# Kernel tuning notes

Hardware: AMD Instinct MI355X
Metric: run time of the kernel (lower is better)

## Reference

```python
import jax, jax.numpy as jnp
import numpy as np

N = 100000   # nodes
E = 800000   # edges
F = 64       # num_features == hidden_dim
D = 64       # hidden_dim
L = 3        # num_gc_layers
NG = 512     # num graphs in batch
BN_EPS = 1e-5


def setup_inputs() -> dict:
    key = jax.random.key(0)
    ks = jax.random.split(key, 16)
    s = 0.05
    return {
        "x": jax.random.normal(ks[0], (N, F), jnp.float32),
        "edge_index": jax.random.randint(ks[1], (2, E), 0, N),
        "batch": jnp.sort(jax.random.randint(ks[2], (N,), 0, NG)),
        "W1": jax.random.normal(ks[3], (L, F, D), jnp.float32) * s,
        "b1": jnp.zeros((L, D), jnp.float32),
        "W2": jax.random.normal(ks[4], (L, D, D), jnp.float32) * s,
        "b2": jnp.zeros((L, D), jnp.float32),
        "gin_eps": jnp.zeros((L,), jnp.float32),
        "gin_bias": jnp.zeros((L, D), jnp.float32),
        "bn_gamma": jnp.ones((L, D), jnp.float32),
        "bn_beta": jnp.zeros((L, D), jnp.float32),
        "Wp1": jax.random.normal(ks[5], (L * D, L * D), jnp.float32) * s,
        "bp1": jnp.zeros((L * D,), jnp.float32),
        "Wp2": jax.random.normal(ks[6], (L * D, L * D), jnp.float32) * s,
        "bp2": jnp.zeros((L * D,), jnp.float32),
    }


def reference(x, edge_index, batch, W1, b1, W2, b2, gin_eps, gin_bias,
              bn_gamma, bn_beta, Wp1, bp1, Wp2, bp2):
    row, col = edge_index[0], edge_index[1]
    h = x
    xs = []
    for i in range(L):
        # sparse adj @ h : sum over incoming edges (adj[row, col] = 1)
        agg = jax.ops.segment_sum(h[col], row, num_segments=N)
        z = (1.0 + gin_eps[i]) * h + agg
        # GIN internal MLP: Linear -> ReLU -> Linear -> ReLU
        z = jax.nn.relu(z @ W1[i] + b1[i])
        z = jax.nn.relu(z @ W2[i] + b2[i])
        # conv bias + relu (outer F.relu in Encoder is idempotent)
        z = jax.nn.relu(z + gin_bias[i])
        # BatchNorm1d, training mode: batch stats over nodes, biased variance
        mean = jnp.mean(z, axis=0)
        var = jnp.mean(jnp.square(z - mean), axis=0)
        h = (z - mean) * jax.lax.rsqrt(var + BN_EPS) * bn_gamma[i] + bn_beta[i]
        xs.append(h)
    # per-layer global add pool over graphs, then concat -> [NG, L*D]
    pooled = jnp.concatenate(
        [jax.ops.segment_sum(xi, batch, num_segments=NG) for xi in xs], axis=1)
    # projection head: Linear -> ReLU -> Linear
    y = jax.nn.relu(pooled @ Wp1 + bp1) @ Wp2 + bp2
    return y
```

## Files before the change

### kernel.cpp

```cpp
#include <hip/hip_runtime.h>

#define N_NODES 100000
#define N_EDGES 800000
#define DF 64
#define NGRAPH 512
#define LDIM 192
#define BN_EPS 1e-5
#define NTILES 6250
#define GIN_GRID 782
#define NWT (GIN_GRID * 8)
#define NPACKS 12500
#define COLS_CAP 2600000
#define NBUCK 782
#define BCAP 2048
#define NBLK 128
#define CHUNK 6250
#define REGION_CAP 6144
#define PROJ_ROWS 8

typedef __attribute__((ext_vector_type(8))) short bf16x8;
typedef __attribute__((ext_vector_type(4))) float f32x4;

__device__ inline short f2bf(float x) {
    union { float f; unsigned u; } v; v.f = x;
    unsigned r = v.u + 0x7fff + ((v.u >> 16) & 1);
    return (short)(r >> 16);
}
__device__ inline float bf2f(unsigned short u) {
    union { unsigned u; float f; } v; v.u = ((unsigned)u) << 16; return v.f;
}
__device__ inline float bflo(unsigned u) {
    union { unsigned x; float f; } v; v.x = u << 16; return v.f;
}
__device__ inline float bfhi(unsigned u) {
    union { unsigned x; float f; } v; v.x = u & 0xffff0000u; return v.f;
}

__global__ __launch_bounds__(256) void x2bf_kernel(
    const float* __restrict__ x, unsigned short* __restrict__ xb)
{
    int i = blockIdx.x * 256 + threadIdx.x;
    const int total = N_NODES * DF / 8;
    if (i >= total) return;
    const float4* src = (const float4*)(x + (size_t)i * 8);
    float4 a = src[0], b = src[1];
    unsigned short u0 = (unsigned short)f2bf(a.x), u1 = (unsigned short)f2bf(a.y);
    unsigned short u2 = (unsigned short)f2bf(a.z), u3 = (unsigned short)f2bf(a.w);
    unsigned short u4 = (unsigned short)f2bf(b.x), u5 = (unsigned short)f2bf(b.y);
    unsigned short u6 = (unsigned short)f2bf(b.z), u7 = (unsigned short)f2bf(b.w);
    uint4 o;
    o.x = (unsigned)u0 | ((unsigned)u1 << 16);
    o.y = (unsigned)u2 | ((unsigned)u3 << 16);
    o.z = (unsigned)u4 | ((unsigned)u5 << 16);
    o.w = (unsigned)u6 | ((unsigned)u7 << 16);
    ((uint4*)xb)[i] = o;
}

__global__ __launch_bounds__(256) void blk_hist_kernel(
    const int* __restrict__ ei, int* __restrict__ hist)
{
    __shared__ int hh[NBUCK];
    int blk = blockIdx.x, tid = threadIdx.x;
    for (int i = tid; i < NBUCK; i += 256) hh[i] = 0;
    __syncthreads();
    int start = blk * CHUNK, end = min(start + CHUNK, N_EDGES);
    for (int e = start + tid; e < end; e += 256)
        atomicAdd(&hh[ei[e] >> 7], 1);
    __syncthreads();
    for (int i = tid; i < NBUCK; i += 256) hist[blk * NBUCK + i] = hh[i];
}

__global__ __launch_bounds__(NBLK) void blk_scan_kernel(
    const int* __restrict__ hist, int* __restrict__ pos, int* __restrict__ cnt)
{
    __shared__ int buf[NBLK];
    int k = blockIdx.x, b = threadIdx.x;
    int v = hist[b * NBUCK + k];
    buf[b] = v;
    __syncthreads();
    for (int o = 1; o < NBLK; o <<= 1) {
        int t = (b >= o) ? buf[b - o] : 0;
        __syncthreads();
        buf[b] += t;
        __syncthreads();
    }
    pos[b * NBUCK + k] = buf[b] - v;
    if (b == NBLK - 1) cnt[k] = buf[b];
}

__global__ __launch_bounds__(256) void place_kernel(
    const int* __restrict__ ei, const int* __restrict__ pos,
    unsigned* __restrict__ bucketData)
{
    __shared__ int cursor[NBUCK];
    int blk = blockIdx.x, tid = threadIdx.x;
    for (int i = tid; i < NBUCK; i += 256) cursor[i] = pos[blk * NBUCK + i];
    __syncthreads();
    int start = blk * CHUNK, end = min(start + CHUNK, N_EDGES);
    for (int e = start + tid; e < end; e += 256) {
        int r = ei[e];
        int c = ei[N_EDGES + e];
        int k = r >> 7;
        int p = atomicAdd(&cursor[k], 1);
        bucketData[(size_t)k * BCAP + p] = ((unsigned)(r & 127) << 17) | (unsigned)c;
    }
}

__global__ __launch_bounds__(256) void bucket_count_kernel(
    const unsigned* __restrict__ bucketData, const int* __restrict__ cnt,
    int* __restrict__ deg, int* __restrict__ bpad)
{
    __shared__ int rc[128];
    __shared__ int wps[16];
    int b = blockIdx.x, tid = threadIdx.x;
    int rowbase = b << 7;
    int nrows = min(128, N_NODES - rowbase);
    int cntb = cnt[b];
    if (tid < 128) rc[tid] = 0;
    __syncthreads();
    for (int e = tid; e < cntb; e += 256)
        atomicAdd(&rc[bucketData[(size_t)b * BCAP + e] >> 17], 1);
    __syncthreads();
    if (tid < nrows) deg[rowbase + tid] = rc[tid];
    if (tid < 16) {
        int m = 0;
        #pragma unroll
        for (int i = 0; i < 8; ++i) m = max(m, rc[tid * 8 + i]);
        wps[tid] = (m + 1) & ~1;
    }
    __syncthreads();
    if (tid == 0) {
        int s = 0;
        #pragma unroll
        for (int pk = 0; pk < 16; ++pk) s += 8 * wps[pk];
        bpad[b] = s;
    }
}

__global__ __launch_bounds__(1024) void bucket_scan_kernel(
    const int* __restrict__ bpad, int* __restrict__ bbase)
{
    __shared__ int buf[1024];
    int tid = threadIdx.x;
    int own = (tid < NBUCK) ? bpad[tid] : 0;
    buf[tid] = own;
    __syncthreads();
    for (int o = 1; o < 1024; o <<= 1) {
        int t = (tid >= o) ? buf[tid - o] : 0;
        __syncthreads();
        buf[tid] += t;
        __syncthreads();
    }
    if (tid < NBUCK) bbase[tid] = buf[tid] - own;
}

__global__ __launch_bounds__(256) void bucket_emit_kernel(
    const unsigned* __restrict__ bucketData, const int* __restrict__ cnt,
    const int* __restrict__ bbase,
    int* __restrict__ colT, int* __restrict__ offT, int* __restrict__ widT)
{
    __shared__ int rc[128], rcur[128];
    __shared__ int wps[16], pstart[16];
    __shared__ int region[REGION_CAP];
    __shared__ int totalS;
    int b = blockIdx.x, tid = threadIdx.x;
    int rowbase = b << 7;
    int nrows = min(128, N_NODES - rowbase);
    int cntb = cnt[b];
    int base = bbase[b];
    if (tid < 128) { rc[tid] = 0; rcur[tid] = 0; }
    __syncthreads();
    for (int e = tid; e < cntb; e += 256)
        atomicAdd(&rc[bucketData[(size_t)b * BCAP + e] >> 17], 1);
    __syncthreads();
    if (tid < 16) {
        int m = 0;
        #pragma unroll
        for (int i = 0; i < 8; ++i) m = max(m, rc[tid * 8 + i]);
        wps[tid] = (m + 1) & ~1;
    }
    __syncthreads();
    if (tid == 0) {
        int run = 0;
        #pragma unroll
        for (int pk = 0; pk < 16; ++pk) { pstart[pk] = run; run += 8 * wps[pk]; }
        totalS = run;
    }
    __syncthreads();
    int total = totalS;
    for (int e = tid; e < cntb; e += 256) {
        unsigned p = bucketData[(size_t)b * BCAP + e];
        int lr = p >> 17;
        int c = p & 0x1FFFF;
        int slot = atomicAdd(&rcur[lr], 1);
        int pk = lr >> 3, g = lr & 7;
        region[pstart[pk] + slot * 8 + g] = c * DF;
    }
    __syncthreads();
    for (int i = tid; i < nrows; i += 256) {
        int pk = i >> 3, g = i & 7;
        int wp = wps[pk];
        int sent = (rowbase + i) * DF;
        for (int slot = rc[i]; slot < wp; ++slot)
            region[pstart[pk] + slot * 8 + g] = sent;
    }
    __syncthreads();
    for (int k = tid; k < total; k += 256) colT[base + k] = region[k];
    if (tid < 16 && tid * 8 < nrows) {
        offT[b * 16 + tid] = base + pstart[tid];
        widT[b * 16 + tid] = wps[tid];
    }
}

__global__ __launch_bounds__(256) void gstart_kernel(
    const int* __restrict__ batch, int* __restrict__ gstart,
    float* __restrict__ idsc, float* __restrict__ idsh)
{
    int g = blockIdx.x * 256 + threadIdx.x;
    if (g < 64) { idsc[g] = 1.0f; idsh[g] = 0.0f; }
    if (g > NGRAPH) return;
    if (g == NGRAPH) { gstart[g] = N_NODES; return; }
    int lo = 0, hi = N_NODES;
    while (lo < hi) {
        int mid = (lo + hi) >> 1;
        if (batch[mid] < g) lo = mid + 1; else hi = mid;
    }
    gstart[g] = lo;
}

__global__ __launch_bounds__(256) void pack_w_kernel(
    const float* __restrict__ W1, const float* __restrict__ W2,
    short* __restrict__ Wpk)
{
    int u = blockIdx.x;
    int layer = u >> 1, gm = u & 1;
    const float* W = (gm ? W2 : W1) + layer * 4096;
    short* dst = Wpk + u * 4096;
    for (int idx = threadIdx.x; idx < 4096; idx += 256) {
        int i = idx & 7;
        int l = (idx >> 3) & 63;
        int rest = idx >> 9;
        int kt = rest & 1, nt = rest >> 1;
        int k = kt * 32 + (l >> 4) * 8 + i;
        int n = nt * 16 + (l & 15);
        dst[idx] = f2bf(W[k * 64 + n]);
    }
}

__global__ __launch_bounds__(512) void gin_layer_kernel(
    const unsigned short* __restrict__ zpb,
    const float* __restrict__ sc_in,
    const float* __restrict__ sh_in,
    const int* __restrict__ offT,
    const int* __restrict__ widT,
    const int* __restrict__ deg,
    const int* __restrict__ colT,
    unsigned short* __restrict__ zout,
    const short* __restrict__ Wpk,
    const float* __restrict__ b1,
    const float* __restrict__ b2,
    const float* __restrict__ gin_eps,
    const float* __restrict__ gin_bias,
    float* __restrict__ part_s,
    float* __restrict__ part_q)
{
    __shared__ __align__(16) short Wp1s[4096];
    __shared__ __align__(16) short Wp2s[4096];
    __shared__ __align__(16) short zs[8][16 * 80];

    int tid = threadIdx.x;
    {
        const short4* s1 = (const short4*)Wpk;
        const short4* s2 = (const short4*)(Wpk + 4096);
        short4* d1 = (short4*)Wp1s;
        short4* d2 = (short4*)Wp2s;
        for (int i = tid; i < 1024; i += 512) { d1[i] = s1[i]; d2[i] = s2[i]; }
    }

    int w = tid >> 6, l = tid & 63;
    int lr = l & 15;
    int lk = l >> 4;
    int g8 = l >> 3;
    int j8 = l & 7;
    float epsf = 1.0f + gin_eps[0];
    float b1f[4], b2f[4], gbf[4];
    #pragma unroll
    for (int nt = 0; nt < 4; ++nt) {
        b1f[nt] = b1[nt * 16 + lr];
        b2f[nt] = b2[nt * 16 + lr];
        gbf[nt] = gin_bias[nt * 16 + lr];
    }
    float4 sca = *(const float4*)&sc_in[j8 * 8];
    float4 scb = *(const float4*)&sc_in[j8 * 8 + 4];
    float4 sha = *(const float4*)&sh_in[j8 * 8];
    float4 shb = *(const float4*)&sh_in[j8 * 8 + 4];
    float ssum[4] = {0, 0, 0, 0}, sq[4] = {0, 0, 0, 0};
    short* zw = zs[w];
    __syncthreads();

    int t = blockIdx.x * 8 + w;
    bool active = t < NTILES;

    if (active) {
        #pragma unroll
        for (int half = 0; half < 2; ++half) {
            int p = t * 2 + half;
            int nP0 = p * 8;
            int sP = __builtin_amdgcn_readfirstlane(offT[p]);
            int wP = __builtin_amdgcn_readfirstlane(widT[p]);
            float acc[8];
            #pragma unroll
            for (int i = 0; i < 8; ++i) acc[i] = 0.0f;
            #pragma unroll 1
            for (int it = 0; it < wP; it += 2) {
                int co0 = colT[sP + it * 8 + g8];
                int co1 = colT[sP + it * 8 + 8 + g8];
                uint4 v0 = *(const uint4*)(zpb + co0 + j8 * 8);
                uint4 v1 = *(const uint4*)(zpb + co1 + j8 * 8);
                acc[0] += bflo(v0.x) + bflo(v1.x);
                acc[1] += bfhi(v0.x) + bfhi(v1.x);
                acc[2] += bflo(v0.y) + bflo(v1.y);
                acc[3] += bfhi(v0.y) + bfhi(v1.y);
                acc[4] += bflo(v0.z) + bflo(v1.z);
                acc[5] += bfhi(v0.z) + bfhi(v1.z);
                acc[6] += bflo(v0.w) + bflo(v1.w);
                acc[7] += bfhi(v0.w) + bfhi(v1.w);
            }
            int node = nP0 + g8;
            int d = deg[node];
            uint4 hv = *(const uint4*)(zpb + node * DF + j8 * 8);
            float hn[8] = { bflo(hv.x), bfhi(hv.x), bflo(hv.y), bfhi(hv.y),
                            bflo(hv.z), bfhi(hv.z), bflo(hv.w), bfhi(hv.w) };
            float np = (float)(wP - d);
            float em = epsf - np;
            float dh = epsf + (float)d;
            float scv[8] = { sca.x, sca.y, sca.z, sca.w, scb.x, scb.y, scb.z, scb.w };
            float shv[8] = { sha.x, sha.y, sha.z, sha.w, shb.x, shb.y, shb.z, shb.w };
            unsigned short us[8];
            #pragma unroll
            for (int i = 0; i < 8; ++i) {
                float zf = scv[i] * (em * hn[i] + acc[i]) + dh * shv[i];
                us[i] = (unsigned short)f2bf(zf);
            }
            uint4 zpk;
            zpk.x = (unsigned)us[0] | ((unsigned)us[1] << 16);
            zpk.y = (unsigned)us[2] | ((unsigned)us[3] << 16);
            zpk.z = (unsigned)us[4] | ((unsigned)us[5] << 16);
            zpk.w = (unsigned)us[6] | ((unsigned)us[7] << 16);
            *(uint4*)&zw[(half * 8 + g8) * 80 + j8 * 8] = zpk;
        }

        {
            bf16x8 a0 = *(const bf16x8*)&zw[lr * 80 + lk * 8];
            bf16x8 a1 = *(const bf16x8*)&zw[lr * 80 + 32 + lk * 8];
            #pragma unroll
            for (int nt = 0; nt < 4; ++nt) {
                f32x4 acc = {0.f, 0.f, 0.f, 0.f};
                bf16x8 bb0 = *(const bf16x8*)&Wp1s[((nt * 2 + 0) * 64 + l) * 8];
                bf16x8 bb1 = *(const bf16x8*)&Wp1s[((nt * 2 + 1) * 64 + l) * 8];
                acc = __builtin_amdgcn_mfma_f32_16x16x32_bf16(a0, bb0, acc, 0, 0, 0);
                acc = __builtin_amdgcn_mfma_f32_16x16x32_bf16(a1, bb1, acc, 0, 0, 0);
                #pragma unroll
                for (int r = 0; r < 4; ++r) {
                    float v = fmaxf(acc[r] + b1f[nt], 0.0f);
                    zw[(lk * 4 + r) * 80 + nt * 16 + lr] = f2bf(v);
                }
            }
        }

        {
            int n0 = t * 16;
            bf16x8 a0 = *(const bf16x8*)&zw[lr * 80 + lk * 8];
            bf16x8 a1 = *(const bf16x8*)&zw[lr * 80 + 32 + lk * 8];
            #pragma unroll
            for (int nt = 0; nt < 4; ++nt) {
                f32x4 acc = {0.f, 0.f, 0.f, 0.f};
                bf16x8 bb0 = *(const bf16x8*)&Wp2s[((nt * 2 + 0) * 64 + l) * 8];
                bf16x8 bb1 = *(const bf16x8*)&Wp2s[((nt * 2 + 1) * 64 + l) * 8];
                acc = __builtin_amdgcn_mfma_f32_16x16x32_bf16(a0, bb0, acc, 0, 0, 0);
                acc = __builtin_amdgcn_mfma_f32_16x16x32_bf16(a1, bb1, acc, 0, 0, 0);
                #pragma unroll
                for (int r = 0; r < 4; ++r) {
                    float v = fmaxf(fmaxf(acc[r] + b2f[nt], 0.0f) + gbf[nt], 0.0f);
                    unsigned short vb = (unsigned short)f2bf(v);
                    zout[(n0 + lk * 4 + r) * DF + nt * 16 + lr] = vb;
                    float vr = bf2f(vb);
                    ssum[nt] += vr;
                    sq[nt] += vr * vr;
                }
            }
        }
    }

    #pragma unroll
    for (int nt = 0; nt < 4; ++nt) {
        float sv = ssum[nt], qv = sq[nt];
        sv += __shfl_xor(sv, 16, 64); sv += __shfl_xor(sv, 32, 64);
        qv += __shfl_xor(qv, 16, 64); qv += __shfl_xor(qv, 32, 64);
        if (l < 16) {
            part_s[(nt * 16 + l) * NWT + t] = sv;
            part_q[(nt * 16 + l) * NWT + t] = qv;
        }
    }
}

__global__ __launch_bounds__(256) void stat_reduce_kernel(
    const float* __restrict__ part_s, const float* __restrict__ part_q,
    const float* __restrict__ gamma, const float* __restrict__ beta,
    float* __restrict__ scale, float* __restrict__ shift)
{
    __shared__ double rs[4], rq[4];
    int f = blockIdx.x, tid = threadIdx.x;
    double s = 0.0, q = 0.0;
    for (int j = tid; j < NWT; j += 256) {
        s += (double)part_s[f * NWT + j];
        q += (double)part_q[f * NWT + j];
    }
    for (int o = 32; o > 0; o >>= 1) {
        s += __shfl_down(s, o, 64);
        q += __shfl_down(q, o, 64);
    }
    if ((tid & 63) == 0) { rs[tid >> 6] = s; rq[tid >> 6] = q; }
    __syncthreads();
    if (tid == 0) {
        double st = rs[0] + rs[1] + rs[2] + rs[3];
        double qt = rq[0] + rq[1] + rq[2] + rq[3];
        double mean = st / N_NODES;
        double var = qt / N_NODES - mean * mean;
        double inv = (double)gamma[f] / sqrt(var + BN_EPS);
        scale[f] = (float)inv;
        shift[f] = (float)((double)beta[f] - mean * inv);
    }
}

__global__ __launch_bounds__(256) void pool_kernel(
    const unsigned short* __restrict__ z,
    const float* __restrict__ scale,
    const float* __restrict__ shift,
    const int* __restrict__ gstart,
    float* __restrict__ pooled,
    int layerOff)
{
    __shared__ float red[4][64];
    int g = blockIdx.x;
    int tid = threadIdx.x;
    int w = tid >> 6, f = tid & 63;

    int s = gstart[g], e = gstart[g + 1];
    float acc = 0.0f;
    for (int node = s + w; node < e; node += 4)
        acc += bf2f(z[node * DF + f]);
    red[w][f] = acc;
    __syncthreads();
    if (w == 0)
        pooled[g * LDIM + layerOff + f] =
            scale[f] * (red[0][f] + red[1][f] + red[2][f] + red[3][f])
            + (float)(e - s) * shift[f];
}

__global__ __launch_bounds__(192) void proj_fused_kernel(
    const float* __restrict__ in,
    const float* __restrict__ Wp1, const float* __restrict__ bp1,
    const float* __restrict__ Wp2, const float* __restrict__ bp2,
    float* __restrict__ out)
{
    __shared__ float rowS[PROJ_ROWS][LDIM];
    __shared__ float hid[PROJ_ROWS][LDIM];
    int r0 = blockIdx.x * PROJ_ROWS;
    int c = threadIdx.x;
    #pragma unroll
    for (int r = 0; r < PROJ_ROWS; ++r)
        rowS[r][c] = in[(r0 + r) * LDIM + c];
    __syncthreads();

    float acc[PROJ_ROWS];
    float bv = bp1[c];
    #pragma unroll
    for (int r = 0; r < PROJ_ROWS; ++r) acc[r] = bv;
    for (int k = 0; k < LDIM; ++k) {
        float wv = Wp1[k * LDIM + c];
        #pragma unroll
        for (int r = 0; r < PROJ_ROWS; ++r) acc[r] += rowS[r][k] * wv;
    }
    #pragma unroll
    for (int r = 0; r < PROJ_ROWS; ++r) hid[r][c] = fmaxf(acc[r], 0.0f);
    __syncthreads();

    float bv2 = bp2[c];
    #pragma unroll
    for (int r = 0; r < PROJ_ROWS; ++r) acc[r] = bv2;
    for (int k = 0; k < LDIM; ++k) {
        float wv = Wp2[k * LDIM + c];
        #pragma unroll
        for (int r = 0; r < PROJ_ROWS; ++r) acc[r] += hid[r][k] * wv;
    }
    #pragma unroll
    for (int r = 0; r < PROJ_ROWS; ++r)
        out[(r0 + r) * LDIM + c] = acc[r];
}

extern "C" void kernel_launch(void* const* d_in, const int* in_sizes, int n_in,
                              void* d_out, int out_size, void* d_ws, size_t ws_size,
                              hipStream_t stream)
{
    const float* x        = (const float*)d_in[0];
    const int*   ei       = (const int*)d_in[1];
    const int*   batch    = (const int*)d_in[2];
    const float* W1       = (const float*)d_in[3];
    const float* b1       = (const float*)d_in[4];
    const float* W2       = (const float*)d_in[5];
    const float* b2       = (const float*)d_in[6];
    const float* gin_eps  = (const float*)d_in[7];
    const float* gin_bias = (const float*)d_in[8];
    const float* gamma    = (const float*)d_in[9];
    const float* beta     = (const float*)d_in[10];
    const float* Wp1      = (const float*)d_in[11];
    const float* bp1      = (const float*)d_in[12];
    const float* Wp2      = (const float*)d_in[13];
    const float* bp2      = (const float*)d_in[14];
    float* out = (float*)d_out;

    unsigned short* xb    = (unsigned short*)d_ws;
    unsigned short* zbufA = xb + (size_t)N_NODES * DF;
    unsigned short* zbufB = zbufA + (size_t)N_NODES * DF;
    float* pooled = (float*)(zbufB + (size_t)N_NODES * DF);
    float* scale = pooled + (size_t)NGRAPH * LDIM;
    float* shift = scale + 64;
    float* idsc = shift + 64;
    float* idsh = idsc + 64;
    float* part_s = idsh + 64;
    float* part_q = part_s + (size_t)64 * NWT;
    int* gstart = (int*)(part_q + (size_t)64 * NWT);
    int* deg  = gstart + NGRAPH + 1;
    int* offT = deg + N_NODES;
    int* widT = offT + 16 * NBUCK;
    int* colT = widT + 16 * NBUCK;
    int* hist = colT + COLS_CAP;
    int* pos  = hist + NBLK * NBUCK;
    int* cnt  = pos + NBLK * NBUCK;
    int* bpad = cnt + NBUCK;
    int* bbase = bpad + NBUCK;
    unsigned* bucketData = (unsigned*)(bbase + NBUCK);
    short* Wpk = (short*)(bucketData + (size_t)NBUCK * BCAP);

    x2bf_kernel<<<(N_NODES * DF / 8 + 255) / 256, 256, 0, stream>>>(x, xb);
    blk_hist_kernel<<<NBLK, 256, 0, stream>>>(ei, hist);
    blk_scan_kernel<<<NBUCK, NBLK, 0, stream>>>(hist, pos, cnt);
    place_kernel<<<NBLK, 256, 0, stream>>>(ei, pos, bucketData);
    bucket_count_kernel<<<NBUCK, 256, 0, stream>>>(bucketData, cnt, deg, bpad);
    bucket_scan_kernel<<<1, 1024, 0, stream>>>(bpad, bbase);
    bucket_emit_kernel<<<NBUCK, 256, 0, stream>>>(bucketData, cnt, bbase,
                                                  colT, offT, widT);
    gstart_kernel<<<3, 256, 0, stream>>>(batch, gstart, idsc, idsh);
    pack_w_kernel<<<6, 256, 0, stream>>>(W1, W2, Wpk);

    unsigned short* zbuf[2] = {zbufA, zbufB};
    const unsigned short* zprev = xb;
    const float* sc_in = idsc;
    const float* sh_in = idsh;
    for (int l = 0; l < 3; ++l) {
        unsigned short* zcur = zbuf[l & 1];
        gin_layer_kernel<<<GIN_GRID, 512, 0, stream>>>(
            zprev, sc_in, sh_in, offT, widT, deg, colT, zcur,
            Wpk + (size_t)l * 8192,
            b1 + l * 64, b2 + l * 64, gin_eps + l, gin_bias + l * 64,
            part_s, part_q);

        stat_reduce_kernel<<<64, 256, 0, stream>>>(
            part_s, part_q, gamma + l * 64, beta + l * 64, scale, shift);

        pool_kernel<<<NGRAPH, 256, 0, stream>>>(
            zcur, scale, shift, gstart, pooled, l * 64);

        zprev = zcur;
        sc_in = scale;
        sh_in = shift;
    }

    proj_fused_kernel<<<NGRAPH / PROJ_ROWS, LDIM, 0, stream>>>(
        pooled, Wp1, bp1, Wp2, bp2, out);
}
```

Before: 265.5 us.

## Fuse global add pooling into GIN layer via atomics and prefetch gather loads

Drops the separate per-layer pool kernel. Each GIN tile now accumulates raw pre-BN sums per graph into the pooled buffer with atomic adds, doing one add per wave when all 16 nodes of the tile belong to the same graph. The BN affine is applied later in the projection kernel as scale*sum + count*shift. The edge gather loop is also software-pipelined so the next pair of neighbor rows loads before the current pair is accumulated. In exchange it adds atomic contention on pooled, a memset, and extra batch reads in the hot kernel.

```diff
diff --git a/kernel.cpp b/kernel.cpp
--- a/kernel.cpp
+++ b/kernel.cpp
@@ -9,7 +9,6 @@
 #define NTILES 6250
 #define GIN_GRID 782
 #define NWT (GIN_GRID * 8)
-#define NPACKS 12500
 #define COLS_CAP 2600000
 #define NBUCK 782
 #define BCAP 2048
@@ -255,7 +254,10 @@
     const int* __restrict__ widT,
     const int* __restrict__ deg,
     const int* __restrict__ colT,
+    const int* __restrict__ batch,
     unsigned short* __restrict__ zout,
+    float* __restrict__ pooled,
+    int lOff,
     const short* __restrict__ Wpk,
     const float* __restrict__ b1,
     const float* __restrict__ b2,
@@ -300,8 +302,20 @@
 
     int t = blockIdx.x * 8 + w;
     bool active = t < NTILES;
+    int n0 = t * 16;
+    int g0 = 0;
+    bool uni = true;
+    int gr[4];
 
     if (active) {
+        g0 = batch[n0];
+        int gl = batch[n0 + (l & 15)];
+        uni = __all(gl == g0);
+        if (!uni) {
+            #pragma unroll
+            for (int r = 0; r < 4; ++r) gr[r] = batch[n0 + lk * 4 + r];
+        }
+
         #pragma unroll
         for (int half = 0; half < 2; ++half) {
             int p = t * 2 + half;
@@ -311,12 +325,27 @@
             float acc[8];
             #pragma unroll
             for (int i = 0; i < 8; ++i) acc[i] = 0.0f;
-            #pragma unroll 1
-            for (int it = 0; it < wP; it += 2) {
-                int co0 = colT[sP + it * 8 + g8];
-                int co1 = colT[sP + it * 8 + 8 + g8];
+            if (wP > 0) {
+                int co0 = colT[sP + g8];
+                int co1 = colT[sP + 8 + g8];
                 uint4 v0 = *(const uint4*)(zpb + co0 + j8 * 8);
                 uint4 v1 = *(const uint4*)(zpb + co1 + j8 * 8);
+                #pragma unroll 1
+                for (int it = 2; it < wP; it += 2) {
+                    int cn0 = colT[sP + it * 8 + g8];
+                    int cn1 = colT[sP + it * 8 + 8 + g8];
+                    uint4 nv0 = *(const uint4*)(zpb + cn0 + j8 * 8);
+                    uint4 nv1 = *(const uint4*)(zpb + cn1 + j8 * 8);
+                    acc[0] += bflo(v0.x) + bflo(v1.x);
+                    acc[1] += bfhi(v0.x) + bfhi(v1.x);
+                    acc[2] += bflo(v0.y) + bflo(v1.y);
+                    acc[3] += bfhi(v0.y) + bfhi(v1.y);
+                    acc[4] += bflo(v0.z) + bflo(v1.z);
+                    acc[5] += bfhi(v0.z) + bfhi(v1.z);
+                    acc[6] += bflo(v0.w) + bflo(v1.w);
+                    acc[7] += bfhi(v0.w) + bfhi(v1.w);
+                    v0 = nv0; v1 = nv1;
+                }
                 acc[0] += bflo(v0.x) + bflo(v1.x);
                 acc[1] += bfhi(v0.x) + bfhi(v1.x);
                 acc[2] += bflo(v0.y) + bflo(v1.y);
@@ -369,7 +398,6 @@
         }
 
         {
-            int n0 = t * 16;
             bf16x8 a0 = *(const bf16x8*)&zw[lr * 80 + lk * 8];
             bf16x8 a1 = *(const bf16x8*)&zw[lr * 80 + 32 + lk * 8];
             #pragma unroll
@@ -387,20 +415,29 @@
                     float vr = bf2f(vb);
                     ssum[nt] += vr;
                     sq[nt] += vr * vr;
+                    if (!uni)
+                        unsafeAtomicAdd(&pooled[gr[r] * LDIM + lOff + nt * 16 + lr], vr);
                 }
             }
         }
     }
 
+    float svv[4];
     #pragma unroll
     for (int nt = 0; nt < 4; ++nt) {
         float sv = ssum[nt], qv = sq[nt];
         sv += __shfl_xor(sv, 16, 64); sv += __shfl_xor(sv, 32, 64);
         qv += __shfl_xor(qv, 16, 64); qv += __shfl_xor(qv, 32, 64);
+        svv[nt] = sv;
         if (l < 16) {
             part_s[(nt * 16 + l) * NWT + t] = sv;
             part_q[(nt * 16 + l) * NWT + t] = qv;
         }
+    }
+    if (active && uni && l < 16) {
+        #pragma unroll
+        for (int nt = 0; nt < 4; ++nt)
+            unsafeAtomicAdd(&pooled[g0 * LDIM + lOff + nt * 16 + l], svv[nt]);
     }
 }
 
@@ -433,33 +470,10 @@
     }
 }
 
-__global__ __launch_bounds__(256) void pool_kernel(
-    const unsigned short* __restrict__ z,
-    const float* __restrict__ scale,
-    const float* __restrict__ shift,
+__global__ __launch_bounds__(192) void proj_fused_kernel(
+    const float* __restrict__ praw,
+    const float* __restrict__ scale3, const float* __restrict__ shift3,
     const int* __restrict__ gstart,
-    float* __restrict__ pooled,
-    int layerOff)
-{
-    __shared__ float red[4][64];
-    int g = blockIdx.x;
-    int tid = threadIdx.x;
-    int w = tid >> 6, f = tid & 63;
-
-    int s = gstart[g], e = gstart[g + 1];
-    float acc = 0.0f;
-    for (int node = s + w; node < e; node += 4)
-        acc += bf2f(z[node * DF + f]);
-    red[w][f] = acc;
-    __syncthreads();
-    if (w == 0)
-        pooled[g * LDIM + layerOff + f] =
-            scale[f] * (red[0][f] + red[1][f] + red[2][f] + red[3][f])
-            + (float)(e - s) * shift[f];
-}
-
-__global__ __launch_bounds__(192) void proj_fused_kernel(
-    const float* __restrict__ in,
     const float* __restrict__ Wp1, const float* __restrict__ bp1,
     const float* __restrict__ Wp2, const float* __restrict__ bp2,
     float* __restrict__ out)
@@ -468,9 +482,13 @@
     __shared__ float hid[PROJ_ROWS][LDIM];
     int r0 = blockIdx.x * PROJ_ROWS;
     int c = threadIdx.x;
+    float scc = scale3[c], shc = shift3[c];
     #pragma unroll
-    for (int r = 0; r < PROJ_ROWS; ++r)
-        rowS[r][c] = in[(r0 + r) * LDIM + c];
+    for (int r = 0; r < PROJ_ROWS; ++r) {
+        int g = r0 + r;
+        float cntg = (float)(gstart[g + 1] - gstart[g]);
+        rowS[r][c] = scc * praw[g * LDIM + c] + cntg * shc;
+    }
     __syncthreads();
 
     float acc[PROJ_ROWS];
@@ -524,9 +542,9 @@
     unsigned short* zbufA = xb + (size_t)N_NODES * DF;
     unsigned short* zbufB = zbufA + (size_t)N_NODES * DF;
     float* pooled = (float*)(zbufB + (size_t)N_NODES * DF);
-    float* scale = pooled + (size_t)NGRAPH * LDIM;
-    float* shift = scale + 64;
-    float* idsc = shift + 64;
+    float* scale3 = pooled + (size_t)NGRAPH * LDIM;
+    float* shift3 = scale3 + LDIM;
+    float* idsc = shift3 + LDIM;
     float* idsh = idsc + 64;
     float* part_s = idsh + 64;
     float* part_q = part_s + (size_t)64 * NWT;
@@ -543,6 +561,7 @@
     unsigned* bucketData = (unsigned*)(bbase + NBUCK);
     short* Wpk = (short*)(bucketData + (size_t)NBUCK * BCAP);
 
+    hipMemsetAsync(pooled, 0, (size_t)NGRAPH * LDIM * sizeof(float), stream);
     x2bf_kernel<<<(N_NODES * DF / 8 + 255) / 256, 256, 0, stream>>>(x, xb);
     blk_hist_kernel<<<NBLK, 256, 0, stream>>>(ei, hist);
     blk_scan_kernel<<<NBUCK, NBLK, 0, stream>>>(hist, pos, cnt);
@@ -561,22 +580,21 @@
     for (int l = 0; l < 3; ++l) {
         unsigned short* zcur = zbuf[l & 1];
         gin_layer_kernel<<<GIN_GRID, 512, 0, stream>>>(
-            zprev, sc_in, sh_in, offT, widT, deg, colT, zcur,
+            zprev, sc_in, sh_in, offT, widT, deg, colT, batch, zcur,
+            pooled, l * 64,
             Wpk + (size_t)l * 8192,
             b1 + l * 64, b2 + l * 64, gin_eps + l, gin_bias + l * 64,
             part_s, part_q);
 
         stat_reduce_kernel<<<64, 256, 0, stream>>>(
-            part_s, part_q, gamma + l * 64, beta + l * 64, scale, shift);
-
-        pool_kernel<<<NGRAPH, 256, 0, stream>>>(
-            zcur, scale, shift, gstart, pooled, l * 64);
+            part_s, part_q, gamma + l * 64, beta + l * 64,
+            scale3 + l * 64, shift3 + l * 64);
 
         zprev = zcur;
-        sc_in = scale;
-        sh_in = shift;
+        sc_in = scale3 + l * 64;
+        sh_in = shift3 + l * 64;
     }
 
     proj_fused_kernel<<<NGRAPH / PROJ_ROWS, LDIM, 0, stream>>>(
-        pooled, Wp1, bp1, Wp2, bp2, out);
-}
+        pooled, scale3, shift3, gstart, Wp1, bp1, Wp2, bp2, out);
+}
```

Measured after the change: 240.7 us, median of 2. 1.1x faster.
